# Optimization experiments

Hardware: AMD Instinct MI355X
Metric: run time of the kernel (lower is better)

Reference implementation:

```python
import jax, jax.numpy as jnp
import numpy as np

V = 25000
E = 100000
NODE_IN = 74
EDGE_IN = 12
OUT = 64
EHID = 128
NUM_STEPS = 6


def setup_inputs() -> dict:
    key = jax.random.key(0)
    ks = jax.random.split(key, 12)
    s = 0.05
    node_feats = jax.random.normal(ks[0], (V, NODE_IN), dtype=jnp.float32)
    edge_feats = jax.random.normal(ks[1], (E, EDGE_IN), dtype=jnp.float32)
    src = jax.random.randint(ks[2], (E,), 0, V)
    dst = jax.random.randint(ks[3], (E,), 0, V)
    # project_node_feats: Linear(node_in, out)
    Wp = jax.random.normal(ks[4], (NODE_IN, OUT), dtype=jnp.float32) * s
    bp = jnp.zeros((OUT,), dtype=jnp.float32)
    # edge network: Linear(edge_in, ehid) -> ReLU -> Linear(ehid, out*out)
    We1 = jax.random.normal(ks[5], (EDGE_IN, EHID), dtype=jnp.float32) * s
    be1 = jnp.zeros((EHID,), dtype=jnp.float32)
    We2 = jax.random.normal(ks[6], (EHID, OUT * OUT), dtype=jnp.float32) * s
    be2 = jnp.zeros((OUT * OUT,), dtype=jnp.float32)
    # NNConv output bias
    bias = jnp.zeros((OUT,), dtype=jnp.float32)
    return {
        "node_feats": node_feats, "edge_feats": edge_feats,
        "src": src, "dst": dst,
        "Wp": Wp, "bp": bp,
        "We1": We1, "be1": be1, "We2": We2, "be2": be2,
        "bias": bias,
    }


def reference(node_feats, edge_feats, src, dst, Wp, bp, We1, be1, We2, be2, bias):
    # project node features
    h = jax.nn.relu(node_feats @ Wp + bp)  # [V, OUT]
    # per-edge weight matrices (same every step -> hoist out of loop)
    ew = jax.nn.relu(edge_feats @ We1 + be1) @ We2 + be2  # [E, OUT*OUT]
    ew = ew.reshape(E, OUT, OUT)
    for _ in range(NUM_STEPS):
        # gather src node feats, batched matvec, scatter-sum to dst
        msg = jnp.einsum('ei,eio->eo', h[src], ew)  # [E, OUT]
        agg = jax.ops.segment_sum(msg, dst, num_segments=V)  # [V, OUT]
        h = jax.nn.relu(agg + bias)
    return h
```

## Files before the change

kernel.cpp:

```cpp
#include <hip/hip_runtime.h>
#include <hip/hip_bf16.h>

#define Vn 25000
#define En 100000
#define NODE_IN 74
#define EDGE_IN 12
#define OUTD 64
#define EHID 128
#define NUM_STEPS 6

#define HPAD 68

typedef __attribute__((ext_vector_type(8))) _Float16 half8;
typedef __attribute__((ext_vector_type(4))) float floatx4;

__global__ void proj_kernel(const float* __restrict__ node,
                            const float* __restrict__ Wp,
                            const float* __restrict__ bp,
                            float* __restrict__ h) {
  __shared__ float nf[NODE_IN];
  int v = blockIdx.x;
  int o = threadIdx.x;
  for (int i = o; i < NODE_IN; i += 64) nf[i] = node[(size_t)v * NODE_IN + i];
  __syncthreads();
  float acc = bp[o];
  for (int i = 0; i < NODE_IN; ++i) acc = fmaf(nf[i], Wp[i * OUTD + o], acc);
  h[(size_t)v * OUTD + o] = fmaxf(acc, 0.0f);
}

__global__ void edge_kernel(const float* __restrict__ ef,
                            const float* __restrict__ We1,
                            const float* __restrict__ be1,
                            _Float16* __restrict__ f) {
  __shared__ float es[EDGE_IN];
  int e = blockIdx.x;
  int k = threadIdx.x;
  if (k < EDGE_IN) es[k] = ef[(size_t)e * EDGE_IN + k];
  __syncthreads();
  float acc = be1[k];
  for (int j = 0; j < EDGE_IN; ++j) acc = fmaf(es[j], We1[j * EHID + k], acc);
  f[(size_t)e * EHID + k] = (_Float16)fmaxf(acc, 0.0f);
}

__global__ void w2r_kernel(const float* __restrict__ We2,
                           _Float16* __restrict__ w2s) {
  int g = blockIdx.x * 256 + threadIdx.x;
  int j = g & 7;
  int quad = (g >> 3) & 3;
  int l15 = (g >> 5) & 15;
  int s = (g >> 9) & 3;
  int wv = (g >> 11) & 3;
  int i = g >> 13;
  int k = s * 32 + quad * 8 + j;
  int col = i * 64 + wv * 16 + l15;
  w2s[g] = (_Float16)We2[(size_t)k * (OUTD * OUTD) + col];
}

__global__ __launch_bounds__(256, 2) void msg_kernel(
    const float* __restrict__ h,
    const _Float16* __restrict__ f,
    const _Float16* __restrict__ w2s,
    const int* __restrict__ src,
    const int* __restrict__ dst,
    const float* __restrict__ be2,
    float* __restrict__ agg) {
  __shared__ __align__(16) float smem[8192];
  __shared__ int s_dst[64];

  const int tid = threadIdx.x;
  const int wv = tid >> 6;
  const int lane = tid & 63;
  const int quad = lane >> 4;
  const int l15 = lane & 15;
  const int e0 = blockIdx.x * 64;

  if (tid < 64) {
    int e = e0 + tid;
    s_dst[tid] = (e < En) ? dst[e] : -1;
  }
  {
    int e = tid & 63;
    int ib = tid >> 6;
    int eg = e0 + e;
    int sv = (eg < En) ? src[eg] : 0;
    const float4* hp = reinterpret_cast<const float4*>(h + (size_t)sv * OUTD + ib * 16);
    for (int c = 0; c < 4; ++c) {
      float4 val = hp[c];
      int i4 = ib * 16 + c * 4;
      smem[(i4 + 0) * HPAD + e] = val.x;
      smem[(i4 + 1) * HPAD + e] = val.y;
      smem[(i4 + 2) * HPAD + e] = val.z;
      smem[(i4 + 3) * HPAD + e] = val.w;
    }
  }
  __syncthreads();

  half8 afr[4][4];
#pragma unroll
  for (int t = 0; t < 4; ++t) {
    int e = e0 + t * 16 + l15;
    if (e >= En) e = En - 1;
    const _Float16* fr = f + (size_t)e * EHID + quad * 8;
#pragma unroll
    for (int s = 0; s < 4; ++s)
      afr[t][s] = *reinterpret_cast<const half8*>(fr + s * 32);
  }

  const _Float16* w2l = w2s + l15 * 32 + quad * 8;

#define LOADB4(B, II, SS)                                                   \
  {                                                                         \
    const _Float16* p_ = w2l + (size_t)(II) * 8192 + (SS) * 512;            \
    B[0] = *reinterpret_cast<const half8*>(p_);                             \
    B[1] = *reinterpret_cast<const half8*>(p_ + 2048);                      \
    B[2] = *reinterpret_cast<const half8*>(p_ + 4096);                      \
    B[3] = *reinterpret_cast<const half8*>(p_ + 6144);                      \
  }

  floatx4 acc[4][4];
  const floatx4 zero4 = (floatx4){0.f, 0.f, 0.f, 0.f};
#pragma unroll
  for (int t = 0; t < 4; ++t)
#pragma unroll
    for (int c = 0; c < 4; ++c) acc[t][c] = zero4;

  half8 b0[4], b1[4];
  const int ibase = wv * 16;
  LOADB4(b0, ibase, 0);

#define SSTEP(SS, CURB, NXTB, NI, NS)                                         \
  {                                                                           \
    LOADB4(NXTB, NI, NS);                                                     \
    _Pragma("unroll") for (int t = 0; t < 4; ++t) {                           \
      half8 as = afr[t][SS] * hb[t];                                          \
      acc[t][0] = __builtin_amdgcn_mfma_f32_16x16x32_f16(as, CURB[0], acc[t][0], 0, 0, 0); \
      acc[t][1] = __builtin_amdgcn_mfma_f32_16x16x32_f16(as, CURB[1], acc[t][1], 0, 0, 0); \
      acc[t][2] = __builtin_amdgcn_mfma_f32_16x16x32_f16(as, CURB[2], acc[t][2], 0, 0, 0); \
      acc[t][3] = __builtin_amdgcn_mfma_f32_16x16x32_f16(as, CURB[3], acc[t][3], 0, 0, 0); \
    }                                                                         \
  }

  for (int ii = 0; ii < 16; ++ii) {
    int iv = ibase + ii;
    half8 hb[4];
#pragma unroll
    for (int t = 0; t < 4; ++t) {
      _Float16 hf = (_Float16)smem[iv * HPAD + t * 16 + l15];
      hb[t] = (half8){hf, hf, hf, hf, hf, hf, hf, hf};
    }
    int nxi = (ii == 15) ? iv : iv + 1;
    SSTEP(0, b0, b1, iv, 1);
    SSTEP(1, b1, b0, iv, 2);
    SSTEP(2, b0, b1, iv, 3);
    SSTEP(3, b1, b0, nxi, 0);
  }

  if (wv == 0) {
#pragma unroll
    for (int s = 0; s < 2; ++s) {
      half8 b2f[4];
#pragma unroll
      for (int c = 0; c < 4; ++c) {
        half8 v;
#pragma unroll
        for (int j = 0; j < 8; ++j)
          v[j] = (_Float16)be2[(s * 32 + quad * 8 + j) * 64 + c * 16 + l15];
        b2f[c] = v;
      }
#pragma unroll
      for (int t = 0; t < 4; ++t) {
        half8 ha;
#pragma unroll
        for (int j = 0; j < 8; ++j)
          ha[j] = (_Float16)smem[(s * 32 + quad * 8 + j) * HPAD + t * 16 + l15];
#pragma unroll
        for (int c = 0; c < 4; ++c)
          acc[t][c] = __builtin_amdgcn_mfma_f32_16x16x32_f16(ha, b2f[c], acc[t][c], 0, 0, 0);
      }
    }
  }

  floatx4* scv = reinterpret_cast<floatx4*>(smem);

#define ST1(TG)                                                           \
  _Pragma("unroll") for (int c = 0; c < 4; ++c)                           \
      scv[wv * 512 + (((TG) & 1) * 4 + c) * 64 + lane] = acc[TG][c];
#define LD1(TK)                                                           \
  _Pragma("unroll") for (int c = 0; c < 4; ++c)                           \
      acc[TK][c] += scv[(wv ^ 1) * 512 + (((TK) & 1) * 4 + c) * 64 + lane];
#define ST2(TG)                                                           \
  _Pragma("unroll") for (int c = 0; c < 4; ++c)                           \
      scv[wv * 512 + c * 64 + lane] = acc[TG][c];
#define LD2(TK)                                                           \
  _Pragma("unroll") for (int c = 0; c < 4; ++c)                           \
      acc[TK][c] += scv[(wv ^ 2) * 512 + c * 64 + lane];
#define SCAT(TF)                                                          \
  {                                                                       \
    int rb = (TF) * 16 + quad * 4;                                        \
    _Pragma("unroll") for (int c = 0; c < 4; ++c) {                       \
      int col = c * 16 + l15;                                             \
      _Pragma("unroll") for (int r = 0; r < 4; ++r) {                     \
        int d = s_dst[rb + r];                                            \
        if (d >= 0) atomicAdd(&agg[(size_t)d * OUTD + col], acc[TF][c][r]); \
      }                                                                   \
    }                                                                     \
  }

  __syncthreads();
  if ((wv & 1) == 0) { ST1(2); ST1(3); } else { ST1(0); ST1(1); }
  __syncthreads();
  if ((wv & 1) == 0) { LD1(0); LD1(1); } else { LD1(2); LD1(3); }
  __syncthreads();
  if (wv == 0) { ST2(1); } else if (wv == 1) { ST2(3); }
  else if (wv == 2) { ST2(0); } else { ST2(2); }
  __syncthreads();
  if (wv == 0) { LD2(0); SCAT(0); }
  else if (wv == 1) { LD2(2); SCAT(2); }
  else if (wv == 2) { LD2(1); SCAT(1); }
  else { LD2(3); SCAT(3); }
}

__global__ void update_kernel(float* __restrict__ agg,
                              const float* __restrict__ bias,
                              float* __restrict__ hout,
                              float* __restrict__ dout, int last) {
  int g = blockIdx.x * 256 + threadIdx.x;
  if (g >= Vn * OUTD) return;
  float v = agg[g];
  agg[g] = 0.0f;
  float r = fmaxf(v + bias[g & 63], 0.0f);
  hout[g] = r;
  if (last) dout[g] = r;
}

extern "C" void kernel_launch(void* const* d_in, const int* in_sizes, int n_in,
                              void* d_out, int out_size, void* d_ws, size_t ws_size,
                              hipStream_t stream) {
  const float* node = (const float*)d_in[0];
  const float* edge = (const float*)d_in[1];
  const int* src = (const int*)d_in[2];
  const int* dst = (const int*)d_in[3];
  const float* Wp   = (const float*)d_in[4];
  const float* bp   = (const float*)d_in[5];
  const float* We1  = (const float*)d_in[6];
  const float* be1  = (const float*)d_in[7];
  const float* We2  = (const float*)d_in[8];
  const float* be2  = (const float*)d_in[9];
  const float* bias = (const float*)d_in[10];
  float* out = (float*)d_out;

  char* ws = (char*)d_ws;
  float* agg = (float*)(ws);
  float* h_a = (float*)(ws + 6400000);
  float* h_b = (float*)(ws + 12800000);
  _Float16* f   = (_Float16*)(ws + 19200000);
  _Float16* w2s = (_Float16*)(ws + 44800000);

  hipMemsetAsync(agg, 0, (size_t)Vn * OUTD * sizeof(float), stream);
  proj_kernel<<<Vn, 64, 0, stream>>>(node, Wp, bp, h_a);
  edge_kernel<<<En, 128, 0, stream>>>(edge, We1, be1, f);
  w2r_kernel<<<(OUTD * OUTD * EHID) / 256, 256, 0, stream>>>(We2, w2s);

  float* hin = h_a;
  float* hout = h_b;
  for (int s = 0; s < NUM_STEPS; ++s) {
    msg_kernel<<<(En + 63) / 64, 256, 0, stream>>>(hin, f, w2s, src, dst, be2, agg);
    update_kernel<<<(Vn * OUTD + 255) / 256, 256, 0, stream>>>(
        agg, bias, hout, out, s == NUM_STEPS - 1);
    float* t = hin; hin = hout; hout = t;
  }
}
```

Measured before the change: 998.4 us.

## Split msg_kernel work by edge-tile half and input half to cut registers

Each wave now handles two of the four 16-edge tiles and half of the 64 input dims, instead of all four tiles and a quarter of the inputs. This halves the accumulator and A-fragment registers, allowing launch bounds of 4 blocks per SIMD. Shared memory shrinks to the h tile only, and the cross-wave reduction drops from two stages to one. The trade-off is that each wave now streams twice as many W2 B-fragments per block, raising global and L2 traffic for the weight loads.

```diff
diff --git a/kernel.cpp b/kernel.cpp
--- a/kernel.cpp
+++ b/kernel.cpp
@@ -56,7 +56,7 @@
   w2s[g] = (_Float16)We2[(size_t)k * (OUTD * OUTD) + col];
 }
 
-__global__ __launch_bounds__(256, 2) void msg_kernel(
+__global__ __launch_bounds__(256, 4) void msg_kernel(
     const float* __restrict__ h,
     const _Float16* __restrict__ f,
     const _Float16* __restrict__ w2s,
@@ -64,11 +64,13 @@
     const int* __restrict__ dst,
     const float* __restrict__ be2,
     float* __restrict__ agg) {
-  __shared__ __align__(16) float smem[8192];
+  __shared__ __align__(16) float smem[64 * HPAD];
   __shared__ int s_dst[64];
 
   const int tid = threadIdx.x;
   const int wv = tid >> 6;
+  const int th = wv & 1;
+  const int ih = wv >> 1;
   const int lane = tid & 63;
   const int quad = lane >> 4;
   const int l15 = lane & 15;
@@ -95,15 +97,15 @@
   }
   __syncthreads();
 
-  half8 afr[4][4];
-#pragma unroll
-  for (int t = 0; t < 4; ++t) {
-    int e = e0 + t * 16 + l15;
+  half8 afr[2][4];
+#pragma unroll
+  for (int tl = 0; tl < 2; ++tl) {
+    int e = e0 + (th * 2 + tl) * 16 + l15;
     if (e >= En) e = En - 1;
     const _Float16* fr = f + (size_t)e * EHID + quad * 8;
 #pragma unroll
     for (int s = 0; s < 4; ++s)
-      afr[t][s] = *reinterpret_cast<const half8*>(fr + s * 32);
+      afr[tl][s] = *reinterpret_cast<const half8*>(fr + s * 32);
   }
 
   const _Float16* w2l = w2s + l15 * 32 + quad * 8;
@@ -117,45 +119,45 @@
     B[3] = *reinterpret_cast<const half8*>(p_ + 6144);                      \
   }
 
-  floatx4 acc[4][4];
+  floatx4 acc[2][4];
   const floatx4 zero4 = (floatx4){0.f, 0.f, 0.f, 0.f};
 #pragma unroll
-  for (int t = 0; t < 4; ++t)
-#pragma unroll
-    for (int c = 0; c < 4; ++c) acc[t][c] = zero4;
+  for (int tl = 0; tl < 2; ++tl)
+#pragma unroll
+    for (int c = 0; c < 4; ++c) acc[tl][c] = zero4;
 
   half8 b0[4], b1[4];
-  const int ibase = wv * 16;
+  const int ibase = ih * 32;
   LOADB4(b0, ibase, 0);
 
 #define SSTEP(SS, CURB, NXTB, NI, NS)                                         \
   {                                                                           \
     LOADB4(NXTB, NI, NS);                                                     \
-    _Pragma("unroll") for (int t = 0; t < 4; ++t) {                           \
-      half8 as = afr[t][SS] * hb[t];                                          \
-      acc[t][0] = __builtin_amdgcn_mfma_f32_16x16x32_f16(as, CURB[0], acc[t][0], 0, 0, 0); \
-      acc[t][1] = __builtin_amdgcn_mfma_f32_16x16x32_f16(as, CURB[1], acc[t][1], 0, 0, 0); \
-      acc[t][2] = __builtin_amdgcn_mfma_f32_16x16x32_f16(as, CURB[2], acc[t][2], 0, 0, 0); \
-      acc[t][3] = __builtin_amdgcn_mfma_f32_16x16x32_f16(as, CURB[3], acc[t][3], 0, 0, 0); \
+    _Pragma("unroll") for (int tl = 0; tl < 2; ++tl) {                        \
+      half8 as = afr[tl][SS] * hb[tl];                                        \
+      acc[tl][0] = __builtin_amdgcn_mfma_f32_16x16x32_f16(as, CURB[0], acc[tl][0], 0, 0, 0); \
+      acc[tl][1] = __builtin_amdgcn_mfma_f32_16x16x32_f16(as, CURB[1], acc[tl][1], 0, 0, 0); \
+      acc[tl][2] = __builtin_amdgcn_mfma_f32_16x16x32_f16(as, CURB[2], acc[tl][2], 0, 0, 0); \
+      acc[tl][3] = __builtin_amdgcn_mfma_f32_16x16x32_f16(as, CURB[3], acc[tl][3], 0, 0, 0); \
     }                                                                         \
   }
 
-  for (int ii = 0; ii < 16; ++ii) {
+  for (int ii = 0; ii < 32; ++ii) {
     int iv = ibase + ii;
-    half8 hb[4];
-#pragma unroll
-    for (int t = 0; t < 4; ++t) {
-      _Float16 hf = (_Float16)smem[iv * HPAD + t * 16 + l15];
-      hb[t] = (half8){hf, hf, hf, hf, hf, hf, hf, hf};
+    half8 hb[2];
+#pragma unroll
+    for (int tl = 0; tl < 2; ++tl) {
+      _Float16 hf = (_Float16)smem[iv * HPAD + (th * 2 + tl) * 16 + l15];
+      hb[tl] = (half8){hf, hf, hf, hf, hf, hf, hf, hf};
     }
-    int nxi = (ii == 15) ? iv : iv + 1;
+    int nxi = (ii == 31) ? iv : iv + 1;
     SSTEP(0, b0, b1, iv, 1);
     SSTEP(1, b1, b0, iv, 2);
     SSTEP(2, b0, b1, iv, 3);
     SSTEP(3, b1, b0, nxi, 0);
   }
 
-  if (wv == 0) {
+  if (ih == 0) {
 #pragma unroll
     for (int s = 0; s < 2; ++s) {
       half8 b2f[4];
@@ -168,56 +170,50 @@
         b2f[c] = v;
       }
 #pragma unroll
-      for (int t = 0; t < 4; ++t) {
+      for (int tl = 0; tl < 2; ++tl) {
         half8 ha;
 #pragma unroll
         for (int j = 0; j < 8; ++j)
-          ha[j] = (_Float16)smem[(s * 32 + quad * 8 + j) * HPAD + t * 16 + l15];
+          ha[j] = (_Float16)smem[(s * 32 + quad * 8 + j) * HPAD + (th * 2 + tl) * 16 + l15];
 #pragma unroll
         for (int c = 0; c < 4; ++c)
-          acc[t][c] = __builtin_amdgcn_mfma_f32_16x16x32_f16(ha, b2f[c], acc[t][c], 0, 0, 0);
+          acc[tl][c] = __builtin_amdgcn_mfma_f32_16x16x32_f16(ha, b2f[c], acc[tl][c], 0, 0, 0);
       }
     }
   }
 
   floatx4* scv = reinterpret_cast<floatx4*>(smem);
 
-#define ST1(TG)                                                           \
-  _Pragma("unroll") for (int c = 0; c < 4; ++c)                           \
-      scv[wv * 512 + (((TG) & 1) * 4 + c) * 64 + lane] = acc[TG][c];
-#define LD1(TK)                                                           \
-  _Pragma("unroll") for (int c = 0; c < 4; ++c)                           \
-      acc[TK][c] += scv[(wv ^ 1) * 512 + (((TK) & 1) * 4 + c) * 64 + lane];
-#define ST2(TG)                                                           \
-  _Pragma("unroll") for (int c = 0; c < 4; ++c)                           \
-      scv[wv * 512 + c * 64 + lane] = acc[TG][c];
-#define LD2(TK)                                                           \
-  _Pragma("unroll") for (int c = 0; c < 4; ++c)                           \
-      acc[TK][c] += scv[(wv ^ 2) * 512 + c * 64 + lane];
-#define SCAT(TF)                                                          \
+#define SCAT(TL, T)                                                       \
   {                                                                       \
-    int rb = (TF) * 16 + quad * 4;                                        \
+    int rb = (T) * 16 + quad * 4;                                         \
     _Pragma("unroll") for (int c = 0; c < 4; ++c) {                       \
       int col = c * 16 + l15;                                             \
       _Pragma("unroll") for (int r = 0; r < 4; ++r) {                     \
         int d = s_dst[rb + r];                                            \
-        if (d >= 0) atomicAdd(&agg[(size_t)d * OUTD + col], acc[TF][c][r]); \
+        if (d >= 0) atomicAdd(&agg[(size_t)d * OUTD + col], acc[TL][c][r]); \
       }                                                                   \
     }                                                                     \
   }
 
   __syncthreads();
-  if ((wv & 1) == 0) { ST1(2); ST1(3); } else { ST1(0); ST1(1); }
-  __syncthreads();
-  if ((wv & 1) == 0) { LD1(0); LD1(1); } else { LD1(2); LD1(3); }
-  __syncthreads();
-  if (wv == 0) { ST2(1); } else if (wv == 1) { ST2(3); }
-  else if (wv == 2) { ST2(0); } else { ST2(2); }
-  __syncthreads();
-  if (wv == 0) { LD2(0); SCAT(0); }
-  else if (wv == 1) { LD2(2); SCAT(2); }
-  else if (wv == 2) { LD2(1); SCAT(1); }
-  else { LD2(3); SCAT(3); }
+  if (ih == 0) {
+#pragma unroll
+    for (int c = 0; c < 4; ++c) scv[wv * 256 + c * 64 + lane] = acc[1][c];
+  } else {
+#pragma unroll
+    for (int c = 0; c < 4; ++c) scv[wv * 256 + c * 64 + lane] = acc[0][c];
+  }
+  __syncthreads();
+  if (ih == 0) {
+#pragma unroll
+    for (int c = 0; c < 4; ++c) acc[0][c] += scv[(wv ^ 2) * 256 + c * 64 + lane];
+    SCAT(0, th * 2);
+  } else {
+#pragma unroll
+    for (int c = 0; c < 4; ++c) acc[1][c] += scv[(wv ^ 2) * 256 + c * 64 + lane];
+    SCAT(1, th * 2 + 1);
+  }
 }
 
 __global__ void update_kernel(float* __restrict__ agg,
```

New measurement: 1.448 ms. 45.0% more time.
